# Kernel tuning notes

Measured on AMD Instinct MI355X. Metric: run time of the kernel, lower is better.

## Reference

```python
import jax, jax.numpy as jnp
import numpy as np

LN_EPS = 1e-5

def _layernorm(x, g, b):
    mu = jnp.mean(x, axis=-1, keepdims=True)
    var = jnp.mean(jnp.square(x - mu), axis=-1, keepdims=True)
    return (x - mu) * jax.lax.rsqrt(var + LN_EPS) * g + b


def setup_inputs() -> dict:
    key = jax.random.key(0)
    ks = jax.random.split(key, 8)
    B, N, F = 2, 100000, 128
    E, G = 400000, 10
    EMB, C = 32, 128
    features = jax.random.normal(ks[0], (B, N, F), dtype=jnp.float32)
    edge_index = jax.random.randint(ks[1], (2, E), 0, N, dtype=jnp.int32)
    lengths = jnp.full((G,), N // G, dtype=jnp.int32)
    emb_table = jax.random.normal(ks[2], (128, EMB), dtype=jnp.float32)
    W_in = jax.random.normal(ks[3], (F - 1 + EMB, C), dtype=jnp.float32) * (1.0 / np.sqrt(F - 1 + EMB))
    b_in = jnp.zeros((C,), jnp.float32)
    g_in = jnp.ones((C,), jnp.float32)
    beta_in = jnp.zeros((C,), jnp.float32)
    msg_W = jax.random.normal(ks[4], (3, C, C), dtype=jnp.float32) * (1.0 / np.sqrt(C))
    msg_b = jnp.zeros((3, C), jnp.float32)
    msg_g = jnp.ones((3, C), jnp.float32)
    msg_beta = jnp.zeros((3, C), jnp.float32)
    W_proj = jax.random.normal(ks[5], (C, 1), dtype=jnp.float32) * (1.0 / np.sqrt(C))
    b_proj = jnp.zeros((1,), jnp.float32)
    return {"features": features, "edge_index": edge_index, "lengths": lengths,
            "emb_table": emb_table, "W_in": W_in, "b_in": b_in, "g_in": g_in, "beta_in": beta_in,
            "msg_W": msg_W, "msg_b": msg_b, "msg_g": msg_g, "msg_beta": msg_beta,
            "W_proj": W_proj, "b_proj": b_proj}


def reference(features, edge_index, lengths, emb_table, W_in, b_in, g_in, beta_in,
              msg_W, msg_b, msg_g, msg_beta, W_proj, b_proj):
    B, N, F = features.shape
    rows, cols = edge_index[0], edge_index[1]

    # row-normalized sparse adjacency values (no grad path in original: torch.no_grad)
    ones = jnp.ones(rows.shape[0], dtype=features.dtype)
    deg = jax.ops.segment_sum(ones, rows, num_segments=N)
    vals = 1.0 / jnp.clip(deg, 1.0)[rows]  # [E]
    vals = jax.lax.stop_gradient(vals)

    # embedding input layer
    op = jnp.clip(features[..., 0].astype(jnp.int32), 0, emb_table.shape[0] - 1)  # [B,N]
    x = jnp.concatenate([emb_table[op], features[..., 1:]], axis=-1)  # [B,N,F-1+emb]
    x = _layernorm(jax.nn.silu(x @ W_in + b_in), g_in, beta_in)  # [B,N,C]

    # sparse message passing: agg[i] = sum_j A[i,j] x[j]
    for l in range(msg_W.shape[0]):
        msg = x[:, cols, :] * vals[None, :, None]  # [B,E,C]
        agg = jnp.zeros_like(x).at[:, rows, :].add(msg)  # scatter-sum to rows
        x = _layernorm(jax.nn.silu(agg @ msg_W[l] + msg_b[l]), msg_g[l], msg_beta[l])

    # ragged graph pooling over node axis
    G = lengths.shape[0]
    index = jnp.asarray(np.repeat(np.arange(G), np.asarray(lengths)))  # [N]
    pooled = jax.ops.segment_sum(x.transpose(1, 0, 2), index, num_segments=G)  # [G,B,C]
    runtimes = pooled @ W_proj + b_proj  # [G,B,1]
    return runtimes[..., 0]  # [G,B]
```

## Files before the change

kernel.cpp:

```cpp
#include <hip/hip_runtime.h>
#include <cstddef>

#define LN_EPS 1e-5f
typedef unsigned short u16;
typedef unsigned int u32;
typedef __attribute__((ext_vector_type(8))) short bf16x8;
typedef __attribute__((ext_vector_type(4))) float f32x4;

constexpr int SCAN_T = 256, SCAN_V = 8, SCAN_ELEMS = SCAN_T * SCAN_V;
constexpr int KP = 136;

__device__ inline u16 f2bf(float f) {
    u32 u = __float_as_uint(f);
    u += 0x7FFFu + ((u >> 16) & 1u);
    return (u16)(u >> 16);
}
__device__ inline float bf2f(u16 h) { return __uint_as_float((u32)h << 16); }

__device__ inline void acc_u4(float* a, uint4 u) {
    a[0] += bf2f((u16)(u.x & 0xFFFF)); a[1] += bf2f((u16)(u.x >> 16));
    a[2] += bf2f((u16)(u.y & 0xFFFF)); a[3] += bf2f((u16)(u.y >> 16));
    a[4] += bf2f((u16)(u.z & 0xFFFF)); a[5] += bf2f((u16)(u.z >> 16));
    a[6] += bf2f((u16)(u.w & 0xFFFF)); a[7] += bf2f((u16)(u.w >> 16));
}

__global__ __launch_bounds__(256) void k_deg(const int* __restrict__ rows,
                                             int* __restrict__ deg, int E) {
    int e = blockIdx.x * 256 + threadIdx.x;
    if (e < E) atomicAdd(&deg[rows[e]], 1);
}

__global__ __launch_bounds__(256) void k_invdeg(const int* __restrict__ deg,
                                                float* __restrict__ invdeg, int N) {
    int i = blockIdx.x * 256 + threadIdx.x;
    if (i < N) invdeg[i] = 1.0f / (float)max(deg[i], 1);
}

__global__ __launch_bounds__(SCAN_T) void k_scan1(const int* __restrict__ deg,
                                                  int* __restrict__ row_ptr,
                                                  int* __restrict__ bsum, int N) {
    __shared__ int ts[SCAN_T];
    int t = threadIdx.x;
    int base = blockIdx.x * SCAN_ELEMS;
    int v[SCAN_V];
    int s = 0;
    #pragma unroll
    for (int j = 0; j < SCAN_V; ++j) {
        int i = base + t * SCAN_V + j;
        v[j] = (i < N) ? deg[i] : 0;
        s += v[j];
    }
    ts[t] = s;
    __syncthreads();
    for (int off = 1; off < SCAN_T; off <<= 1) {
        int val = (t >= off) ? ts[t - off] : 0;
        __syncthreads();
        ts[t] += val;
        __syncthreads();
    }
    int excl = (t > 0) ? ts[t - 1] : 0;
    #pragma unroll
    for (int j = 0; j < SCAN_V; ++j) {
        int i = base + t * SCAN_V + j;
        if (i < N) row_ptr[i] = excl;
        excl += v[j];
    }
    if (t == SCAN_T - 1) bsum[blockIdx.x] = ts[SCAN_T - 1];
}

__global__ void k_scan2(int* __restrict__ bsum, int nb, int* __restrict__ row_ptr, int N) {
    int run = 0;
    for (int i = 0; i < nb; ++i) {
        int v = bsum[i];
        bsum[i] = run;
        run += v;
    }
    row_ptr[N] = run;
}

__global__ __launch_bounds__(SCAN_T) void k_scan3(int* __restrict__ row_ptr,
                                                  const int* __restrict__ bsum, int N) {
    int add = bsum[blockIdx.x];
    int base = blockIdx.x * SCAN_ELEMS;
    #pragma unroll
    for (int j = 0; j < SCAN_V; ++j) {
        int i = base + threadIdx.x * SCAN_V + j;
        if (i < N) row_ptr[i] += add;
    }
}

__global__ __launch_bounds__(256) void k_copy_cursor(const int* __restrict__ row_ptr,
                                                     int* __restrict__ cursor, int N) {
    int i = blockIdx.x * 256 + threadIdx.x;
    if (i < N) cursor[i] = row_ptr[i];
}

__global__ __launch_bounds__(256) void k_bucket(const int* __restrict__ rows,
                                                const int* __restrict__ cols,
                                                int* __restrict__ cursor,
                                                int* __restrict__ col_sorted, int E) {
    int e = blockIdx.x * 256 + threadIdx.x;
    if (e < E) {
        int r = rows[e];
        int pos = atomicAdd(&cursor[r], 1);
        col_sorted[pos] = cols[e];
    }
}

__global__ __launch_bounds__(256) void k_wprep(const float* __restrict__ W_in,
                                               const float* __restrict__ msg_W,
                                               u16* __restrict__ Wt_in,
                                               u16* __restrict__ Wt_msg) {
    int idx = blockIdx.x * 256 + threadIdx.x;
    const int t1 = 128 * 128;
    if (idx < t1) {
        int c = idx >> 7, k = idx & 127;
        float v = (k >= 1) ? W_in[(31 + k) * 128 + c] : 0.f;
        Wt_in[idx] = f2bf(v);
    } else {
        idx -= t1;
        if (idx < 3 * 128 * 128) {
            int l = idx / (128 * 128);
            int r = idx & (128 * 128 - 1);
            int c = r >> 7, k = r & 127;
            Wt_msg[idx] = f2bf(msg_W[l * 16384 + k * 128 + c]);
        }
    }
}

__global__ __launch_bounds__(128) void k_eproj(const float* __restrict__ W_in,
                                               const float* __restrict__ emb,
                                               float* __restrict__ E_proj) {
    __shared__ float es[32];
    int op = blockIdx.x, c = threadIdx.x;
    if (c < 32) es[c] = emb[op * 32 + c];
    __syncthreads();
    float s = 0.f;
    #pragma unroll
    for (int j = 0; j < 32; ++j) s = fmaf(es[j], W_in[j * 128 + c], s);
    E_proj[op * 128 + c] = s;
}

__global__ __launch_bounds__(512) void k_input_mfma(
    const float* __restrict__ features, const float* __restrict__ E_proj,
    const u16* __restrict__ Wt,
    const float* __restrict__ bias, const float* __restrict__ gain,
    const float* __restrict__ beta, u16* __restrict__ x, int N, int ntiles)
{
    __shared__ u16 A[64 * KP];
    __shared__ u16 Wl[128 * KP];
    __shared__ int ops[64];
    __shared__ float pS[64][2], pQ[64][2];
    const int tid = threadIdx.x;
    const int lane = tid & 63, w = tid >> 6;
    const int l15 = lane & 15;
    const int kq = (lane >> 4) * 8;
    const int r = tid >> 3, sl = tid & 7;
    const int wr = w & 3, wc = w >> 2;

    for (int i = tid; i < 2048; i += 512) {
        uint4 v = ((const uint4*)Wt)[i];
        *(uint4*)&Wl[(i >> 4) * KP + (i & 15) * 8] = v;
    }

    for (int tile = blockIdx.x; tile < ntiles; tile += gridDim.x) {
        const int node0 = tile * 32;
        {
            int nl = r >> 1, b = r & 1;
            int node = min(node0 + nl, N - 1);
            const float* fr = features + ((size_t)b * N + node) * 128 + sl * 16;
            float4 v0 = ((const float4*)fr)[0];
            float4 v1 = ((const float4*)fr)[1];
            float4 v2 = ((const float4*)fr)[2];
            float4 v3 = ((const float4*)fr)[3];
            if (sl == 0) {
                int op = (int)v0.x;
                op = op < 0 ? 0 : (op > 127 ? 127 : op);
                ops[r] = op;
            }
            u32 pk[8];
            pk[0] = (u32)f2bf(v0.x) | ((u32)f2bf(v0.y) << 16);
            pk[1] = (u32)f2bf(v0.z) | ((u32)f2bf(v0.w) << 16);
            pk[2] = (u32)f2bf(v1.x) | ((u32)f2bf(v1.y) << 16);
            pk[3] = (u32)f2bf(v1.z) | ((u32)f2bf(v1.w) << 16);
            pk[4] = (u32)f2bf(v2.x) | ((u32)f2bf(v2.y) << 16);
            pk[5] = (u32)f2bf(v2.z) | ((u32)f2bf(v2.w) << 16);
            pk[6] = (u32)f2bf(v3.x) | ((u32)f2bf(v3.y) << 16);
            pk[7] = (u32)f2bf(v3.z) | ((u32)f2bf(v3.w) << 16);
            uint4* dst = (uint4*)&A[r * KP + sl * 16];
            dst[0] = make_uint4(pk[0], pk[1], pk[2], pk[3]);
            dst[1] = make_uint4(pk[4], pk[5], pk[6], pk[7]);
        }
        __syncthreads();

        const int arow = wr * 16 + l15;
        bf16x8 a[4];
        #pragma unroll
        for (int kt = 0; kt < 4; ++kt)
            a[kt] = *(const bf16x8*)&A[arow * KP + kt * 32 + kq];
        f32x4 acc[4];
        #pragma unroll
        for (int t = 0; t < 4; ++t) {
            int bcol = wc * 64 + t * 16 + l15;
            f32x4 c4 = {0.f, 0.f, 0.f, 0.f};
            #pragma unroll
            for (int kt = 0; kt < 4; ++kt) {
                bf16x8 b = *(const bf16x8*)&Wl[bcol * KP + kt * 32 + kq];
                c4 = __builtin_amdgcn_mfma_f32_16x16x32_bf16(a[kt], b, c4, 0, 0, 0);
            }
            acc[t] = c4;
        }

        int opr[4];
        #pragma unroll
        for (int i = 0; i < 4; ++i) opr[i] = ops[wr * 16 + (lane >> 4) * 4 + i];

        float s[4] = {0, 0, 0, 0}, sq[4] = {0, 0, 0, 0};
        #pragma unroll
        for (int t = 0; t < 4; ++t) {
            int col = wc * 64 + t * 16 + l15;
            float bt = bias[col];
            #pragma unroll
            for (int i = 0; i < 4; ++i) {
                float aY = acc[t][i] + bt + E_proj[opr[i] * 128 + col];
                float y = aY / (1.0f + __expf(-aY));
                acc[t][i] = y;
                s[i] += y;
                sq[i] = fmaf(y, y, sq[i]);
            }
        }
        #pragma unroll
        for (int m = 1; m <= 8; m <<= 1) {
            #pragma unroll
            for (int i = 0; i < 4; ++i) {
                s[i] += __shfl_xor(s[i], m);
                sq[i] += __shfl_xor(sq[i], m);
            }
        }
        if (l15 == 0) {
            #pragma unroll
            for (int i = 0; i < 4; ++i) {
                int rr = wr * 16 + (lane >> 4) * 4 + i;
                pS[rr][wc] = s[i];
                pQ[rr][wc] = sq[i];
            }
        }
        __syncthreads();

        #pragma unroll
        for (int i = 0; i < 4; ++i) {
            int rr = wr * 16 + (lane >> 4) * 4 + i;
            float st = pS[rr][0] + pS[rr][1];
            float qt = pQ[rr][0] + pQ[rr][1];
            float mu = st * (1.0f / 128.0f);
            float var = qt * (1.0f / 128.0f) - mu * mu;
            float inv = rsqrtf(var + LN_EPS);
            if (node0 + (rr >> 1) < N) {
                u16* xr = x + ((size_t)node0 * 2 + rr) * 128;
                #pragma unroll
                for (int t = 0; t < 4; ++t) {
                    int col = wc * 64 + t * 16 + l15;
                    xr[col] = f2bf((acc[t][i] - mu) * inv * gain[col] + beta[col]);
                }
            }
        }
    }
}

__global__ __launch_bounds__(512) void k_mp_mfma(
    const int* __restrict__ row_ptr, const int* __restrict__ col_sorted,
    const float* __restrict__ invdeg, const u16* __restrict__ xin,
    const u16* __restrict__ Wt, const float* __restrict__ bias,
    const float* __restrict__ gain, const float* __restrict__ beta,
    u16* __restrict__ xout, int N, int ntiles)
{
    __shared__ u16 A[64 * KP];
    __shared__ u16 Wl[128 * KP];
    __shared__ float pS[64][2], pQ[64][2];
    const int tid = threadIdx.x;
    const int lane = tid & 63, w = tid >> 6;
    const int l15 = lane & 15;
    const int kq = (lane >> 4) * 8;
    const int r = tid >> 3, sl = tid & 7;
    const int wr = w & 3, wc = w >> 2;

    for (int i = tid; i < 2048; i += 512) {
        uint4 v = ((const uint4*)Wt)[i];
        *(uint4*)&Wl[(i >> 4) * KP + (i & 15) * 8] = v;
    }

    for (int tile = blockIdx.x; tile < ntiles; tile += gridDim.x) {
        const int node0 = tile * 32;
        {
            int nl = r >> 1, b = r & 1;
            int node = min(node0 + nl, N - 1);
            int e0 = row_ptr[node], e1 = row_ptr[node + 1];
            float sc = invdeg[node];
            const u32* xb = (const u32*)xin + (size_t)b * 64 + sl * 8;
            float fa[16];
            #pragma unroll
            for (int j = 0; j < 16; ++j) fa[j] = 0.f;
            int e = e0;
            for (; e + 2 <= e1; e += 2) {
                int c0 = col_sorted[e], c1 = col_sorted[e + 1];
                const uint4* p0 = (const uint4*)(xb + (size_t)c0 * 128);
                const uint4* p1 = (const uint4*)(xb + (size_t)c1 * 128);
                uint4 u0 = p0[0], u1 = p0[1];
                uint4 w0 = p1[0], w1 = p1[1];
                acc_u4(fa, u0);     acc_u4(fa + 8, u1);
                acc_u4(fa, w0);     acc_u4(fa + 8, w1);
            }
            if (e < e1) {
                const uint4* p0 = (const uint4*)(xb + (size_t)col_sorted[e] * 128);
                uint4 u0 = p0[0], u1 = p0[1];
                acc_u4(fa, u0);     acc_u4(fa + 8, u1);
            }
            u32 pk[8];
            #pragma unroll
            for (int j = 0; j < 8; ++j)
                pk[j] = (u32)f2bf(fa[2 * j] * sc) | ((u32)f2bf(fa[2 * j + 1] * sc) << 16);
            uint4* dst = (uint4*)&A[r * KP + sl * 16];
            dst[0] = make_uint4(pk[0], pk[1], pk[2], pk[3]);
            dst[1] = make_uint4(pk[4], pk[5], pk[6], pk[7]);
        }
        __syncthreads();

        const int arow = wr * 16 + l15;
        bf16x8 a[4];
        #pragma unroll
        for (int kt = 0; kt < 4; ++kt)
            a[kt] = *(const bf16x8*)&A[arow * KP + kt * 32 + kq];
        f32x4 acc[4];
        #pragma unroll
        for (int t = 0; t < 4; ++t) {
            int bcol = wc * 64 + t * 16 + l15;
            f32x4 c4 = {0.f, 0.f, 0.f, 0.f};
            #pragma unroll
            for (int kt = 0; kt < 4; ++kt) {
                bf16x8 bfr = *(const bf16x8*)&Wl[bcol * KP + kt * 32 + kq];
                c4 = __builtin_amdgcn_mfma_f32_16x16x32_bf16(a[kt], bfr, c4, 0, 0, 0);
            }
            acc[t] = c4;
        }

        float s[4] = {0, 0, 0, 0}, sq[4] = {0, 0, 0, 0};
        #pragma unroll
        for (int t = 0; t < 4; ++t) {
            int col = wc * 64 + t * 16 + l15;
            float bt = bias[col];
            #pragma unroll
            for (int i = 0; i < 4; ++i) {
                float aY = acc[t][i] + bt;
                float y = aY / (1.0f + __expf(-aY));
                acc[t][i] = y;
                s[i] += y;
                sq[i] = fmaf(y, y, sq[i]);
            }
        }
        #pragma unroll
        for (int m = 1; m <= 8; m <<= 1) {
            #pragma unroll
            for (int i = 0; i < 4; ++i) {
                s[i] += __shfl_xor(s[i], m);
                sq[i] += __shfl_xor(sq[i], m);
            }
        }
        if (l15 == 0) {
            #pragma unroll
            for (int i = 0; i < 4; ++i) {
                int rr = wr * 16 + (lane >> 4) * 4 + i;
                pS[rr][wc] = s[i];
                pQ[rr][wc] = sq[i];
            }
        }
        __syncthreads();

        #pragma unroll
        for (int i = 0; i < 4; ++i) {
            int rr = wr * 16 + (lane >> 4) * 4 + i;
            float st = pS[rr][0] + pS[rr][1];
            float qt = pQ[rr][0] + pQ[rr][1];
            float mu = st * (1.0f / 128.0f);
            float var = qt * (1.0f / 128.0f) - mu * mu;
            float inv = rsqrtf(var + LN_EPS);
            if (node0 + (rr >> 1) < N) {
                u16* xr = xout + ((size_t)node0 * 2 + rr) * 128;
                #pragma unroll
                for (int t = 0; t < 4; ++t) {
                    int col = wc * 64 + t * 16 + l15;
                    xr[col] = f2bf((acc[t][i] - mu) * inv * gain[col] + beta[col]);
                }
            }
        }
    }
}

__global__ __launch_bounds__(64) void k_pool(
    const u16* __restrict__ x, const int* __restrict__ lengths,
    float* __restrict__ pooled, int N, int B, int G, int SPLIT)
{
    int blk = blockIdx.x;
    int split = blk % SPLIT;
    int gb = blk / SPLIT;
    int b = gb % B, g = gb / B;
    int lane = threadIdx.x;
    int start = 0;
    for (int i = 0; i < g; ++i) start += lengths[i];
    int len = lengths[g];
    int chunk = (len + SPLIT - 1) / SPLIT;
    int n0 = start + split * chunk;
    int n1 = min(start + len, n0 + chunk);
    const u32* xb = (const u32*)x + (size_t)b * 64;
    float sx = 0.f, sy = 0.f;
    int n = n0;
    for (; n + 4 <= n1; n += 4) {
        u32 v0 = xb[(size_t)(n + 0) * 128 + lane];
        u32 v1 = xb[(size_t)(n + 1) * 128 + lane];
        u32 v2 = xb[(size_t)(n + 2) * 128 + lane];
        u32 v3 = xb[(size_t)(n + 3) * 128 + lane];
        sx += bf2f((u16)(v0 & 0xFFFF)) + bf2f((u16)(v1 & 0xFFFF)) +
              bf2f((u16)(v2 & 0xFFFF)) + bf2f((u16)(v3 & 0xFFFF));
        sy += bf2f((u16)(v0 >> 16)) + bf2f((u16)(v1 >> 16)) +
              bf2f((u16)(v2 >> 16)) + bf2f((u16)(v3 >> 16));
    }
    for (; n < n1; ++n) {
        u32 v = xb[(size_t)n * 128 + lane];
        sx += bf2f((u16)(v & 0xFFFF));
        sy += bf2f((u16)(v >> 16));
    }
    if (n1 > n0) {
        atomicAdd(&pooled[(g * B + b) * 128 + lane * 2 + 0], sx);
        atomicAdd(&pooled[(g * B + b) * 128 + lane * 2 + 1], sy);
    }
}

__global__ __launch_bounds__(128) void k_proj(
    const float* __restrict__ pooled, const float* __restrict__ Wp,
    const float* __restrict__ bp, float* __restrict__ out, int GB)
{
    int gb = blockIdx.x;
    int tid = threadIdx.x;
    float v = pooled[gb * 128 + tid] * Wp[tid];
    v += __shfl_down(v, 32);
    v += __shfl_down(v, 16);
    v += __shfl_down(v, 8);
    v += __shfl_down(v, 4);
    v += __shfl_down(v, 2);
    v += __shfl_down(v, 1);
    __shared__ float red[2];
    if ((tid & 63) == 0) red[tid >> 6] = v;
    __syncthreads();
    if (tid == 0) out[gb] = red[0] + red[1] + bp[0];
}

extern "C" void kernel_launch(void* const* d_in, const int* in_sizes, int n_in,
                              void* d_out, int out_size, void* d_ws, size_t ws_size,
                              hipStream_t stream) {
    const float* features = (const float*)d_in[0];
    const int* edge_index = (const int*)d_in[1];
    const int* lengths    = (const int*)d_in[2];
    const float* emb      = (const float*)d_in[3];
    const float* W_in     = (const float*)d_in[4];
    const float* b_in     = (const float*)d_in[5];
    const float* g_in     = (const float*)d_in[6];
    const float* beta_in  = (const float*)d_in[7];
    const float* msg_W    = (const float*)d_in[8];
    const float* msg_b    = (const float*)d_in[9];
    const float* msg_g    = (const float*)d_in[10];
    const float* msg_beta = (const float*)d_in[11];
    const float* W_proj   = (const float*)d_in[12];
    const float* b_proj   = (const float*)d_in[13];
    float* out = (float*)d_out;

    const int E = in_sizes[1] / 2;
    const int G = in_sizes[2];
    const int B = out_size / G;
    const int C = in_sizes[5];
    const int F = 128;
    const int N = in_sizes[0] / (B * F);
    const int M = B * N;
    const int L = in_sizes[9] / C;

    const int* rows = edge_index;
    const int* cols = edge_index + E;

    u16* buf0   = (u16*)d_ws;
    u16* buf1   = buf0 + (size_t)M * 128;
    u16* Wt_in  = buf1 + (size_t)M * 128;
    u16* Wt_msg = Wt_in + 128 * 128;
    float* E_proj = (float*)(Wt_msg + 3 * 128 * 128);
    float* invdeg = E_proj + 128 * 128;
    int*   deg    = (int*)(invdeg + N);
    float* pooled = (float*)(deg + N);
    int*   row_ptr = (int*)(pooled + (size_t)G * B * 128);
    int*   col_sorted = row_ptr + N + 1;
    int*   bsum   = col_sorted + E;

    const int nb_scan = (N + SCAN_ELEMS - 1) / SCAN_ELEMS;
    const int nt32 = (N + 31) / 32;
    const int grid_mp = nt32 < 1024 ? nt32 : 1024;

    {
        int total = 4 * 128 * 128;
        k_wprep<<<(total + 255) / 256, 256, 0, stream>>>(W_in, msg_W, Wt_in, Wt_msg);
        k_eproj<<<128, 128, 0, stream>>>(W_in, emb, E_proj);
    }

    hipMemsetAsync(deg, 0, (size_t)N * sizeof(int), stream);
    k_deg<<<(E + 255) / 256, 256, 0, stream>>>(rows, deg, E);
    k_invdeg<<<(N + 255) / 256, 256, 0, stream>>>(deg, invdeg, N);
    k_scan1<<<nb_scan, SCAN_T, 0, stream>>>(deg, row_ptr, bsum, N);
    k_scan2<<<1, 1, 0, stream>>>(bsum, nb_scan, row_ptr, N);
    k_scan3<<<nb_scan, SCAN_T, 0, stream>>>(row_ptr, bsum, N);
    k_copy_cursor<<<(N + 255) / 256, 256, 0, stream>>>(row_ptr, deg, N);
    k_bucket<<<(E + 255) / 256, 256, 0, stream>>>(rows, cols, deg, col_sorted, E);

    k_input_mfma<<<grid_mp, 512, 0, stream>>>(features, E_proj, Wt_in,
                                              b_in, g_in, beta_in, buf0, N, nt32);

    u16* bufs[2] = {buf0, buf1};
    int cur = 0;
    for (int l = 0; l < L; ++l) {
        k_mp_mfma<<<grid_mp, 512, 0, stream>>>(row_ptr, col_sorted, invdeg,
                                               bufs[cur], Wt_msg + (size_t)l * 128 * 128,
                                               msg_b + (size_t)l * C, msg_g + (size_t)l * C,
                                               msg_beta + (size_t)l * C,
                                               bufs[1 - cur], N, nt32);
        cur = 1 - cur;
    }

    const int SPLIT = 128;
    hipMemsetAsync(pooled, 0, (size_t)G * B * 128 * sizeof(float), stream);
    k_pool<<<G * B * SPLIT, 64, 0, stream>>>(bufs[cur], lengths, pooled, N, B, G, SPLIT);
    k_proj<<<G * B, 128, 0, stream>>>(pooled, W_proj, b_proj, out, G * B);
}
```

Measured before the change: 335.5 us.

## Fuse graph pooling into last message-passing layer epilogue via atomics

The last message-passing layer no longer writes its bf16 node features. Its layernorm outputs are summed per graph and batch directly in registers, reduced across lanes with shuffles, and added to the pooled buffer with atomics. A per-node group index array is built upfront, which removes the separate pooling kernel and the extra read of the final feature matrix. In exchange the layer issues many more float atomics on a small pooled array, which may contend, and summation order becomes nondeterministic.

After: 413.9 us. 1.23x slower.

```diff
diff --git a/kernel.cpp b/kernel.cpp
--- a/kernel.cpp
+++ b/kernel.cpp
@@ -34,6 +34,22 @@
                                                 float* __restrict__ invdeg, int N) {
     int i = blockIdx.x * 256 + threadIdx.x;
     if (i < N) invdeg[i] = 1.0f / (float)max(deg[i], 1);
+}
+
+__global__ void k_gstart(const int* __restrict__ lengths, int* __restrict__ gstart, int G) {
+    int run = 0;
+    for (int i = 0; i < G; ++i) { gstart[i] = run; run += lengths[i]; }
+    gstart[G] = run;
+}
+
+__global__ __launch_bounds__(256) void k_grp(const int* __restrict__ gstart,
+                                             int* __restrict__ grp, int N, int G) {
+    int i = blockIdx.x * 256 + threadIdx.x;
+    if (i < N) {
+        int g = 0;
+        while (g + 1 < G && i >= gstart[g + 1]) ++g;
+        grp[i] = g;
+    }
 }
 
 __global__ __launch_bounds__(SCAN_T) void k_scan1(const int* __restrict__ deg,
@@ -272,7 +288,8 @@
     const float* __restrict__ invdeg, const u16* __restrict__ xin,
     const u16* __restrict__ Wt, const float* __restrict__ bias,
     const float* __restrict__ gain, const float* __restrict__ beta,
-    u16* __restrict__ xout, int N, int ntiles)
+    u16* __restrict__ xout, const int* __restrict__ grp,
+    float* __restrict__ pooled, int fuse, int N, int B, int ntiles)
 {
     __shared__ u16 A[64 * KP];
     __shared__ u16 Wl[128 * KP];
@@ -375,62 +392,88 @@
         }
         __syncthreads();
 
-        #pragma unroll
-        for (int i = 0; i < 4; ++i) {
-            int rr = wr * 16 + (lane >> 4) * 4 + i;
-            float st = pS[rr][0] + pS[rr][1];
-            float qt = pQ[rr][0] + pQ[rr][1];
-            float mu = st * (1.0f / 128.0f);
-            float var = qt * (1.0f / 128.0f) - mu * mu;
-            float inv = rsqrtf(var + LN_EPS);
-            if (node0 + (rr >> 1) < N) {
-                u16* xr = xout + ((size_t)node0 * 2 + rr) * 128;
+        if (!fuse) {
+            #pragma unroll
+            for (int i = 0; i < 4; ++i) {
+                int rr = wr * 16 + (lane >> 4) * 4 + i;
+                float st = pS[rr][0] + pS[rr][1];
+                float qt = pQ[rr][0] + pQ[rr][1];
+                float mu = st * (1.0f / 128.0f);
+                float var = qt * (1.0f / 128.0f) - mu * mu;
+                float inv = rsqrtf(var + LN_EPS);
+                if (node0 + (rr >> 1) < N) {
+                    u16* xr = xout + ((size_t)node0 * 2 + rr) * 128;
+                    #pragma unroll
+                    for (int t = 0; t < 4; ++t) {
+                        int col = wc * 64 + t * 16 + l15;
+                        xr[col] = f2bf((acc[t][i] - mu) * inv * gain[col] + beta[col]);
+                    }
+                }
+            }
+        } else {
+            int nlo = node0 + wr * 8;
+            int g_lo = grp[min(nlo, N - 1)];
+            int g_hi = grp[min(nlo + 7, N - 1)];
+            float gnr[4], btr2[4];
+            #pragma unroll
+            for (int t = 0; t < 4; ++t) {
+                int col = wc * 64 + t * 16 + l15;
+                gnr[t] = gain[col]; btr2[t] = beta[col];
+            }
+            if (g_lo == g_hi) {
+                float sb0[4] = {0, 0, 0, 0}, sb1[4] = {0, 0, 0, 0};
+                #pragma unroll
+                for (int i = 0; i < 4; ++i) {
+                    int rr = wr * 16 + (lane >> 4) * 4 + i;
+                    int node = node0 + (rr >> 1);
+                    float st = pS[rr][0] + pS[rr][1];
+                    float qt = pQ[rr][0] + pQ[rr][1];
+                    float mu = st * (1.0f / 128.0f);
+                    float var = qt * (1.0f / 128.0f) - mu * mu;
+                    float inv = rsqrtf(var + LN_EPS);
+                    float msk = (node < N) ? 1.f : 0.f;
+                    #pragma unroll
+                    for (int t = 0; t < 4; ++t) {
+                        float y = ((acc[t][i] - mu) * inv * gnr[t] + btr2[t]) * msk;
+                        if (i & 1) sb1[t] += y; else sb0[t] += y;
+                    }
+                }
                 #pragma unroll
                 for (int t = 0; t < 4; ++t) {
-                    int col = wc * 64 + t * 16 + l15;
-                    xr[col] = f2bf((acc[t][i] - mu) * inv * gain[col] + beta[col]);
+                    sb0[t] += __shfl_xor(sb0[t], 16); sb1[t] += __shfl_xor(sb1[t], 16);
+                    sb0[t] += __shfl_xor(sb0[t], 32); sb1[t] += __shfl_xor(sb1[t], 32);
                 }
-            }
-        }
-    }
-}
-
-__global__ __launch_bounds__(64) void k_pool(
-    const u16* __restrict__ x, const int* __restrict__ lengths,
-    float* __restrict__ pooled, int N, int B, int G, int SPLIT)
-{
-    int blk = blockIdx.x;
-    int split = blk % SPLIT;
-    int gb = blk / SPLIT;
-    int b = gb % B, g = gb / B;
-    int lane = threadIdx.x;
-    int start = 0;
-    for (int i = 0; i < g; ++i) start += lengths[i];
-    int len = lengths[g];
-    int chunk = (len + SPLIT - 1) / SPLIT;
-    int n0 = start + split * chunk;
-    int n1 = min(start + len, n0 + chunk);
-    const u32* xb = (const u32*)x + (size_t)b * 64;
-    float sx = 0.f, sy = 0.f;
-    int n = n0;
-    for (; n + 4 <= n1; n += 4) {
-        u32 v0 = xb[(size_t)(n + 0) * 128 + lane];
-        u32 v1 = xb[(size_t)(n + 1) * 128 + lane];
-        u32 v2 = xb[(size_t)(n + 2) * 128 + lane];
-        u32 v3 = xb[(size_t)(n + 3) * 128 + lane];
-        sx += bf2f((u16)(v0 & 0xFFFF)) + bf2f((u16)(v1 & 0xFFFF)) +
-              bf2f((u16)(v2 & 0xFFFF)) + bf2f((u16)(v3 & 0xFFFF));
-        sy += bf2f((u16)(v0 >> 16)) + bf2f((u16)(v1 >> 16)) +
-              bf2f((u16)(v2 >> 16)) + bf2f((u16)(v3 >> 16));
-    }
-    for (; n < n1; ++n) {
-        u32 v = xb[(size_t)n * 128 + lane];
-        sx += bf2f((u16)(v & 0xFFFF));
-        sy += bf2f((u16)(v >> 16));
-    }
-    if (n1 > n0) {
-        atomicAdd(&pooled[(g * B + b) * 128 + lane * 2 + 0], sx);
-        atomicAdd(&pooled[(g * B + b) * 128 + lane * 2 + 1], sy);
+                if ((lane >> 4) == 0) {
+                    #pragma unroll
+                    for (int t = 0; t < 4; ++t) {
+                        int col = wc * 64 + t * 16 + l15;
+                        atomicAdd(&pooled[(g_lo * B + 0) * 128 + col], sb0[t]);
+                        atomicAdd(&pooled[(g_lo * B + 1) * 128 + col], sb1[t]);
+                    }
+                }
+            } else {
+                #pragma unroll
+                for (int i = 0; i < 4; ++i) {
+                    int rr = wr * 16 + (lane >> 4) * 4 + i;
+                    int node = node0 + (rr >> 1);
+                    if (node < N) {
+                        float st = pS[rr][0] + pS[rr][1];
+                        float qt = pQ[rr][0] + pQ[rr][1];
+                        float mu = st * (1.0f / 128.0f);
+                        float var = qt * (1.0f / 128.0f) - mu * mu;
+                        float inv = rsqrtf(var + LN_EPS);
+                        int g = grp[node];
+                        int b = rr & 1;
+                        #pragma unroll
+                        for (int t = 0; t < 4; ++t) {
+                            int col = wc * 64 + t * 16 + l15;
+                            float y = (acc[t][i] - mu) * inv * gnr[t] + btr2[t];
+                            atomicAdd(&pooled[(g * B + b) * 128 + col], y);
+                        }
+                    }
+                }
+            }
+        }
     }
 }
 
@@ -495,6 +538,8 @@
     int*   row_ptr = (int*)(pooled + (size_t)G * B * 128);
     int*   col_sorted = row_ptr + N + 1;
     int*   bsum   = col_sorted + E;
+    int*   gstart = bsum + 64;
+    int*   grp    = gstart + G + 1;
 
     const int nb_scan = (N + SCAN_ELEMS - 1) / SCAN_ELEMS;
     const int nt32 = (N + 31) / 32;
@@ -507,6 +552,7 @@
     }
 
     hipMemsetAsync(deg, 0, (size_t)N * sizeof(int), stream);
+    hipMemsetAsync(pooled, 0, (size_t)G * B * 128 * sizeof(float), stream);
     k_deg<<<(E + 255) / 256, 256, 0, stream>>>(rows, deg, E);
     k_invdeg<<<(N + 255) / 256, 256, 0, stream>>>(deg, invdeg, N);
     k_scan1<<<nb_scan, SCAN_T, 0, stream>>>(deg, row_ptr, bsum, N);
@@ -514,6 +560,8 @@
     k_scan3<<<nb_scan, SCAN_T, 0, stream>>>(row_ptr, bsum, N);
     k_copy_cursor<<<(N + 255) / 256, 256, 0, stream>>>(row_ptr, deg, N);
     k_bucket<<<(E + 255) / 256, 256, 0, stream>>>(rows, cols, deg, col_sorted, E);
+    k_gstart<<<1, 1, 0, stream>>>(lengths, gstart, G);
+    k_grp<<<(N + 255) / 256, 256, 0, stream>>>(gstart, grp, N, G);
 
     k_input_mfma<<<grid_mp, 512, 0, stream>>>(features, E_proj, Wt_in,
                                               b_in, g_in, beta_in, buf0, N, nt32);
@@ -521,16 +569,14 @@
     u16* bufs[2] = {buf0, buf1};
     int cur = 0;
     for (int l = 0; l < L; ++l) {
+        int fuse = (l == L - 1) ? 1 : 0;
         k_mp_mfma<<<grid_mp, 512, 0, stream>>>(row_ptr, col_sorted, invdeg,
                                                bufs[cur], Wt_msg + (size_t)l * 128 * 128,
                                                msg_b + (size_t)l * C, msg_g + (size_t)l * C,
                                                msg_beta + (size_t)l * C,
-                                               bufs[1 - cur], N, nt32);
+                                               bufs[1 - cur], grp, pooled, fuse, N, B, nt32);
         cur = 1 - cur;
     }
 
-    const int SPLIT = 128;
-    hipMemsetAsync(pooled, 0, (size_t)G * B * 128 * sizeof(float), stream);
-    k_pool<<<G * B * SPLIT, 64, 0, stream>>>(bufs[cur], lengths, pooled, N, B, G, SPLIT);
     k_proj<<<G * B, 128, 0, stream>>>(pooled, W_proj, b_proj, out, G * B);
 }
```
